# Optimization experiments

Measured on AMD Instinct MI355X. Metric: run time of the kernel, lower is better.

The kernel has to match this reference:

```python
import jax, jax.numpy as jnp
import numpy as np

HIDDEN = 2048
NUM_HEADS = 32
HEAD_DIM = 64
NUM_KV = 8
GROUP = NUM_HEADS // NUM_KV
SCALE = HEAD_DIM ** -0.5
ROPE_BASE = 10000.0


def apply_rope(t):
    # t: [B, H, S, D]; standard half-split rotary embedding
    S, D = t.shape[-2], t.shape[-1]
    inv_freq = 1.0 / (ROPE_BASE ** (jnp.arange(0, D, 2, dtype=jnp.float32) / D))  # [D/2]
    ang = jnp.arange(S, dtype=jnp.float32)[:, None] * inv_freq[None, :]           # [S, D/2]
    cos, sin = jnp.cos(ang), jnp.sin(ang)
    x1, x2 = t[..., : D // 2], t[..., D // 2 :]
    return jnp.concatenate([x1 * cos - x2 * sin, x2 * cos + x1 * sin], axis=-1)


def setup_inputs() -> dict:
    key = jax.random.key(0)
    ks = jax.random.split(key, 10)
    B, S = 2, 2048
    s_in = HIDDEN ** -0.5
    s_o = (NUM_HEADS * HEAD_DIM) ** -0.5
    return {
        "x": jax.random.normal(ks[0], (B, S, HIDDEN), jnp.float32),
        "Wq": jax.random.normal(ks[1], (NUM_HEADS * HEAD_DIM, HIDDEN), jnp.float32) * s_in,
        "bq": jnp.zeros((NUM_HEADS * HEAD_DIM,), jnp.float32),
        "Wk": jax.random.normal(ks[2], (NUM_KV * HEAD_DIM, HIDDEN), jnp.float32) * s_in,
        "bk": jnp.zeros((NUM_KV * HEAD_DIM,), jnp.float32),
        "Wv": jax.random.normal(ks[3], (NUM_KV * HEAD_DIM, HIDDEN), jnp.float32) * s_in,
        "bv": jnp.zeros((NUM_KV * HEAD_DIM,), jnp.float32),
        "Wo": jax.random.normal(ks[4], (HIDDEN, NUM_HEADS * HEAD_DIM), jnp.float32) * s_o,
        "bo": jnp.zeros((HIDDEN,), jnp.float32),
        "key_weights": jax.random.normal(ks[5], (NUM_HEADS,), jnp.float32),
    }


def reference(x, Wq, bq, Wk, bk, Wv, bv, Wo, bo, key_weights):
    B, S, _ = x.shape
    q = (x @ Wq.T + bq).reshape(B, S, NUM_HEADS, HEAD_DIM).transpose(0, 2, 1, 3)
    k = (x @ Wk.T + bk).reshape(B, S, NUM_KV, HEAD_DIM).transpose(0, 2, 1, 3)
    v = (x @ Wv.T + bv).reshape(B, S, NUM_KV, HEAD_DIM).transpose(0, 2, 1, 3)
    q = apply_rope(q)
    k = apply_rope(k)
    # group queries per KV head: [B, kv, g, S, D]
    qg = q.reshape(B, NUM_KV, GROUP, S, HEAD_DIM)
    scores = jnp.einsum("bkgsd,bktd->bkgst", qg, k) * SCALE
    scores = scores * key_weights.reshape(1, NUM_KV, GROUP, 1, 1)
    causal = jnp.tril(jnp.ones((S, S), bool))
    scores = jnp.where(causal, scores, -jnp.inf)
    a = jax.nn.softmax(scores, axis=-1)
    o = jnp.einsum("bkgst,bktd->bkgsd", a, v)  # [B, kv, g, S, D]
    o = o.reshape(B, NUM_HEADS, S, HEAD_DIM).transpose(0, 2, 1, 3).reshape(B, S, NUM_HEADS * HEAD_DIM)
    return o @ Wo.T + bo
```

## Files before the change

kernel.cpp:

```cpp
#include <hip/hip_runtime.h>
#include <stdint.h>

#define S_LEN 2048
#define HID   2048
#define NH    32
#define NKV   8
#define HD    64
#define BATCH 2
#define NROWS (BATCH * S_LEN)
#define QKVN  (NH*HD + 2*NKV*HD)

typedef unsigned short u16;
typedef __bf16 bf16_t;
typedef bf16_t bf16x8 __attribute__((ext_vector_type(8)));
typedef float  f32x4  __attribute__((ext_vector_type(4)));
typedef float  f32x16 __attribute__((ext_vector_type(16)));
typedef u16    u16x8  __attribute__((ext_vector_type(8)));

#define LOG2E 1.4426950408889634f

__device__ __forceinline__ u16 f2bf(float f) {
    union { float f; uint32_t u; } v; v.f = f;
    uint32_t u = v.u;
    return (u16)((u + 0x7fffu + ((u >> 16) & 1u)) >> 16);
}

__device__ __forceinline__ unsigned cvtpk(float a, float b) {
    unsigned r;
    asm("v_cvt_pk_bf16_f32 %0, %1, %2" : "=v"(r) : "v"(a), "v"(b));
    return r;
}

__device__ __forceinline__ void plswap(unsigned &a, unsigned &b) {
    asm volatile("v_permlane32_swap_b32 %0, %1" : "+v"(a), "+v"(b));
}

__device__ __forceinline__ void llds16(const void* g, void* l) {
    __builtin_amdgcn_global_load_lds(
        (const __attribute__((address_space(1))) void*)g,
        (__attribute__((address_space(3))) void*)l,
        16, 0, 0);
}

__device__ __forceinline__ unsigned swz(unsigned row) {
    return ((row ^ (row >> 2)) & 3u) << 4;
}

#define LGKM0() do { asm volatile("s_waitcnt lgkmcnt(0)" ::: "memory"); \
                     __builtin_amdgcn_sched_barrier(0); } while (0)
#define BAR()   __builtin_amdgcn_s_barrier()

#define CBAR(N) do { \
    asm volatile("s_waitcnt vmcnt(" #N ")" ::: "memory"); \
    __builtin_amdgcn_s_barrier(); \
    __builtin_amdgcn_sched_barrier(0); \
} while (0)

#define CVT_GROUPS 2359296
__global__ void prep_all(const float* __restrict__ x, const float* __restrict__ wq,
                         const float* __restrict__ wk, const float* __restrict__ wv,
                         const float* __restrict__ wo,
                         const float* __restrict__ bq, const float* __restrict__ bk,
                         const float* __restrict__ bv,
                         u16* __restrict__ xb, u16* __restrict__ wqkvb, u16* __restrict__ wob,
                         float* __restrict__ rtab, float* __restrict__ bqkv) {
    int e = blockIdx.x * 256 + threadIdx.x;
    if (e < CVT_GROUPS) {
        const float* s; u16* d; int o;
        if (e < 1048576)      { s = x;  d = xb;                 o = e; }
        else if (e < 1572864) { s = wq; d = wqkvb;              o = e - 1048576; }
        else if (e < 1703936) { s = wk; d = wqkvb + 2048*2048;  o = e - 1572864; }
        else if (e < 1835008) { s = wv; d = wqkvb + 2560*2048;  o = e - 1703936; }
        else                  { s = wo; d = wob;                o = e - 1835008; }
        const float4* sp = (const float4*)s;
        float4 a = sp[2*(size_t)o], b = sp[2*(size_t)o + 1];
        u16x8 r;
        r[0]=f2bf(a.x); r[1]=f2bf(a.y); r[2]=f2bf(a.z); r[3]=f2bf(a.w);
        r[4]=f2bf(b.x); r[5]=f2bf(b.y); r[6]=f2bf(b.z); r[7]=f2bf(b.w);
        *(u16x8*)(d + 8*(size_t)o) = r;
    } else if (e < CVT_GROUPS + 65536) {
        int idx = e - CVT_GROUPS;
        int i = idx & 31, s = idx >> 5;
        float invf = exp2f(-(float)i * (13.287712379549449f / 32.0f));
        float ang = (float)s * invf;
        float sn, cs;
        sincosf(ang, &sn, &cs);
        rtab[idx] = cs;
        rtab[S_LEN*32 + idx] = sn;
    } else if (e < CVT_GROUPS + 65536 + QKVN) {
        int i = e - CVT_GROUPS - 65536;
        bqkv[i] = (i < 2048) ? bq[i] : (i < 2560 ? bk[i - 2048] : bv[i - 2560]);
    }
}


__global__ __launch_bounds__(256, 2) void gemm_qkv(
    const u16* __restrict__ A, const u16* __restrict__ Bw,
    const float* __restrict__ bias, const float* __restrict__ rtab,
    const float* __restrict__ kw,
    u16* __restrict__ qpk, u16* __restrict__ kpk, u16* __restrict__ vlin)
{
    const int M = NROWS, N = QKVN, K = HID;
    const int nbn = N >> 8;
    const int nwg = (M >> 7) * nbn;
    int wg = blockIdx.x;
    wg = (wg & 7) * (nwg >> 3) + (wg >> 3);
    const int bm = wg / nbn, bn = wg % nbn;
    const int brow = bm << 7, bcol = bn << 8;

    __shared__ u16 sbuf[3][12288];

    const int t = threadIdx.x;
    const int lane = t & 63, wid = t >> 6;
    const int wr = wid >> 1, wn = wid & 1;
    const int lq = lane & 31, hi = lane >> 5;

    auto stageA = [&](int kt, int bi) {
        const int k0 = kt << 5;
        #pragma unroll
        for (int i = 0; i < 2; ++i) {
            const unsigned off = ((unsigned)t << 4) + ((unsigned)i << 12);
            const unsigned row = off >> 6;
            const unsigned scb = (off & 63) ^ swz(row);
            llds16(A + (size_t)(brow + row) * K + (k0 + (scb >> 1)), &sbuf[bi][0] + (off >> 1));
        }
        {
            const unsigned off = ((unsigned)t << 4);
            const unsigned row = off >> 6;
            const unsigned scb = (off & 63) ^ swz(row);
            llds16(Bw + (size_t)(bcol + row) * K + (k0 + (scb >> 1)), &sbuf[bi][4096] + (off >> 1));
        }
    };
    auto stageB = [&](int kt, int bi) {
        const int k0 = kt << 5;
        #pragma unroll
        for (int i = 1; i < 4; ++i) {
            const unsigned off = ((unsigned)t << 4) + ((unsigned)i << 12);
            const unsigned row = off >> 6;
            const unsigned scb = (off & 63) ^ swz(row);
            llds16(Bw + (size_t)(bcol + row) * K + (k0 + (scb >> 1)), &sbuf[bi][4096] + (off >> 1));
        }
    };

    f32x16 acc[2][4] = {};
    const int nk = K >> 5;

    stageA(0, 0); stageB(0, 0);
    stageA(1, 1); stageB(1, 1);
    asm volatile("s_waitcnt vmcnt(6)" ::: "memory");
    BAR();

    int cur = 0, st2 = 2;
    for (int kt = 0; kt < nk; ++kt) {
        const char* sA = (const char*)&sbuf[cur][0];
        const char* sB = (const char*)&sbuf[cur][4096];
        bf16x8 af[4], bfv[8];
        #pragma unroll
        for (int mt = 0; mt < 2; ++mt)
            #pragma unroll
            for (int s = 0; s < 2; ++s) {
                const unsigned row = wr*64 + mt*32 + lq;
                af[mt*2+s] = *(const bf16x8*)(sA + row*64 + ((unsigned)(32*s + 16*hi) ^ swz(row)));
            }
        #pragma unroll
        for (int nt = 0; nt < 2; ++nt)
            #pragma unroll
            for (int s = 0; s < 2; ++s) {
                const unsigned row = wn*128 + nt*32 + lq;
                bfv[nt*2+s] = *(const bf16x8*)(sB + row*64 + ((unsigned)(32*s + 16*hi) ^ swz(row)));
            }
        if (kt + 2 < nk) stageA(kt + 2, st2);
        BAR();
        LGKM0();
        __builtin_amdgcn_s_setprio(1);
        #pragma unroll
        for (int mt = 0; mt < 2; ++mt)
            #pragma unroll
            for (int nt = 0; nt < 2; ++nt)
                #pragma unroll
                for (int s = 0; s < 2; ++s)
                    acc[mt][nt] = __builtin_amdgcn_mfma_f32_32x32x16_bf16(af[mt*2+s], bfv[nt*2+s], acc[mt][nt], 0, 0, 0);
        __builtin_amdgcn_s_setprio(0);
        BAR();
        #pragma unroll
        for (int nt = 2; nt < 4; ++nt)
            #pragma unroll
            for (int s = 0; s < 2; ++s) {
                const unsigned row = wn*128 + nt*32 + lq;
                bfv[nt*2+s] = *(const bf16x8*)(sB + row*64 + ((unsigned)(32*s + 16*hi) ^ swz(row)));
            }
        if (kt + 2 < nk) stageB(kt + 2, st2);
        BAR();
        LGKM0();
        __builtin_amdgcn_s_setprio(1);
        #pragma unroll
        for (int mt = 0; mt < 2; ++mt)
            #pragma unroll
            for (int nt = 2; nt < 4; ++nt)
                #pragma unroll
                for (int s = 0; s < 2; ++s)
                    acc[mt][nt] = __builtin_amdgcn_mfma_f32_32x32x16_bf16(af[mt*2+s], bfv[nt*2+s], acc[mt][nt], 0, 0, 0);
        __builtin_amdgcn_s_setprio(0);
        if (kt + 2 < nk) {
            asm volatile("s_waitcnt vmcnt(6)" ::: "memory");
            BAR();
        } else if (kt + 1 < nk) {
            asm volatile("s_waitcnt vmcnt(0)" ::: "memory");
            BAR();
        }
        cur = (cur == 2) ? 0 : cur + 1;
        st2 = (st2 == 2) ? 0 : st2 + 1;
    }

    const int rowb = brow + wr*64;
    #pragma unroll
    for (int hg = 0; hg < 2; ++hg) {
        const int c64 = bcol + wn*128 + hg*64;
        const int hb  = c64 >> 6;
        if (hb < 40) {
            const bool isQ = hb < 32;
            const float sc = isQ ? (0.125f * LOG2E * kw[hb]) : 1.0f;
            u16* dst = isQ ? qpk : kpk;
            const int nheads = isQ ? 32 : 8;
            const int hloc = isQ ? hb : (hb - 32);
            const float b1 = bias[c64 + lq];
            const float b2 = bias[c64 + 32 + lq];
            #pragma unroll
            for (int mt = 0; mt < 2; ++mt) {
                #pragma unroll
                for (int r = 0; r < 16; ++r) {
                    const int row = rowb + mt*32 + (r & 3) + 8*(r >> 2) + 4*hi;
                    const int s = row & (S_LEN - 1);
                    const int bb = row >> 11;
                    const float x1 = acc[mt][2*hg][r] + b1;
                    const float x2 = acc[mt][2*hg + 1][r] + b2;
                    const float c = rtab[s*32 + lq];
                    const float sn = rtab[S_LEN*32 + s*32 + lq];
                    const size_t base = ((size_t)(bb*nheads + hloc)) * (S_LEN*64) + (size_t)s*64;
                    dst[base + lq]      = f2bf((x1*c - x2*sn) * sc);
                    dst[base + lq + 32] = f2bf((x2*c + x1*sn) * sc);
                }
            }
        } else {
            #pragma unroll
            for (int nn = 0; nn < 2; ++nn) {
                const int col = c64 + nn*32 + lq;
                const float bv = bias[col];
                #pragma unroll
                for (int mt = 0; mt < 2; ++mt)
                    #pragma unroll
                    for (int r = 0; r < 16; ++r) {
                        const int row = rowb + mt*32 + (r & 3) + 8*(r >> 2) + 4*hi;
                        vlin[(size_t)row * 512 + (col - 2560)] = f2bf(acc[mt][2*hg + nn][r] + bv);
                    }
            }
        }
    }
}

__global__ __launch_bounds__(256, 2) void gemm_bt(
    const u16* __restrict__ A, const u16* __restrict__ Bw,
    const float* __restrict__ bias, float* __restrict__ C,
    int M, int N, int K)
{
    const int nbn = N >> 8;
    const int nwg = (M >> 7) * nbn;
    int wg = blockIdx.x;
    wg = (wg & 7) * (nwg >> 3) + (wg >> 3);
    const int bm = wg / nbn, bn = wg % nbn;
    const int brow = bm << 7, bcol = bn << 8;

    __shared__ u16 sbuf[3][12288];

    const int t = threadIdx.x;
    const int lane = t & 63, wid = t >> 6;
    const int wr = wid >> 1, wn = wid & 1;
    const int lq = lane & 31, hi = lane >> 5;

    auto stageA = [&](int kt, int bi) {
        const int k0 = kt << 5;
        #pragma unroll
        for (int i = 0; i < 2; ++i) {
            const unsigned off = ((unsigned)t << 4) + ((unsigned)i << 12);
            const unsigned row = off >> 6;
            const unsigned scb = (off & 63) ^ swz(row);
            llds16(A + (size_t)(brow + row) * K + (k0 + (scb >> 1)), &sbuf[bi][0] + (off >> 1));
        }
        {
            const unsigned off = ((unsigned)t << 4);
            const unsigned row = off >> 6;
            const unsigned scb = (off & 63) ^ swz(row);
            llds16(Bw + (size_t)(bcol + row) * K + (k0 + (scb >> 1)), &sbuf[bi][4096] + (off >> 1));
        }
    };
    auto stageB = [&](int kt, int bi) {
        const int k0 = kt << 5;
        #pragma unroll
        for (int i = 1; i < 4; ++i) {
            const unsigned off = ((unsigned)t << 4) + ((unsigned)i << 12);
            const unsigned row = off >> 6;
            const unsigned scb = (off & 63) ^ swz(row);
            llds16(Bw + (size_t)(bcol + row) * K + (k0 + (scb >> 1)), &sbuf[bi][4096] + (off >> 1));
        }
    };

    f32x16 acc[2][4] = {};
    const int nk = K >> 5;

    stageA(0, 0); stageB(0, 0);
    stageA(1, 1); stageB(1, 1);
    asm volatile("s_waitcnt vmcnt(6)" ::: "memory");
    BAR();

    int cur = 0, st2 = 2;
    for (int kt = 0; kt < nk; ++kt) {
        const char* sA = (const char*)&sbuf[cur][0];
        const char* sB = (const char*)&sbuf[cur][4096];
        bf16x8 af[4], bfv[8];
        #pragma unroll
        for (int mt = 0; mt < 2; ++mt)
            #pragma unroll
            for (int s = 0; s < 2; ++s) {
                const unsigned row = wr*64 + mt*32 + lq;
                af[mt*2+s] = *(const bf16x8*)(sA + row*64 + ((unsigned)(32*s + 16*hi) ^ swz(row)));
            }
        #pragma unroll
        for (int nt = 0; nt < 2; ++nt)
            #pragma unroll
            for (int s = 0; s < 2; ++s) {
                const unsigned row = wn*128 + nt*32 + lq;
                bfv[nt*2+s] = *(const bf16x8*)(sB + row*64 + ((unsigned)(32*s + 16*hi) ^ swz(row)));
            }
        if (kt + 2 < nk) stageA(kt + 2, st2);
        BAR();
        LGKM0();
        __builtin_amdgcn_s_setprio(1);
        #pragma unroll
        for (int mt = 0; mt < 2; ++mt)
            #pragma unroll
            for (int nt = 0; nt < 2; ++nt)
                #pragma unroll
                for (int s = 0; s < 2; ++s)
                    acc[mt][nt] = __builtin_amdgcn_mfma_f32_32x32x16_bf16(af[mt*2+s], bfv[nt*2+s], acc[mt][nt], 0, 0, 0);
        __builtin_amdgcn_s_setprio(0);
        BAR();
        #pragma unroll
        for (int nt = 2; nt < 4; ++nt)
            #pragma unroll
            for (int s = 0; s < 2; ++s) {
                const unsigned row = wn*128 + nt*32 + lq;
                bfv[nt*2+s] = *(const bf16x8*)(sB + row*64 + ((unsigned)(32*s + 16*hi) ^ swz(row)));
            }
        if (kt + 2 < nk) stageB(kt + 2, st2);
        BAR();
        LGKM0();
        __builtin_amdgcn_s_setprio(1);
        #pragma unroll
        for (int mt = 0; mt < 2; ++mt)
            #pragma unroll
            for (int nt = 2; nt < 4; ++nt)
                #pragma unroll
                for (int s = 0; s < 2; ++s)
                    acc[mt][nt] = __builtin_amdgcn_mfma_f32_32x32x16_bf16(af[mt*2+s], bfv[nt*2+s], acc[mt][nt], 0, 0, 0);
        __builtin_amdgcn_s_setprio(0);
        if (kt + 2 < nk) {
            asm volatile("s_waitcnt vmcnt(6)" ::: "memory");
            BAR();
        } else if (kt + 1 < nk) {
            asm volatile("s_waitcnt vmcnt(0)" ::: "memory");
            BAR();
        }
        cur = (cur == 2) ? 0 : cur + 1;
        st2 = (st2 == 2) ? 0 : st2 + 1;
    }

    #pragma unroll
    for (int mt = 0; mt < 2; ++mt)
        #pragma unroll
        for (int nt = 0; nt < 4; ++nt) {
            const int col = bcol + wn*128 + nt*32 + lq;
            const float bv = bias[col];
            #pragma unroll
            for (int r = 0; r < 16; ++r) {
                const int row = brow + wr*64 + mt*32 + (r & 3) + 8*(r >> 2) + 4*hi;
                C[(size_t)row * N + col] = acc[mt][nt][r] + bv;
            }
        }
}

__global__ void pack_vt(const u16* __restrict__ vlin, u16* __restrict__ vtb) {
    __shared__ u16 tile[64][67];
    const int st = blockIdx.x;
    const int bk = blockIdx.y;
    const int t = threadIdx.x;
    const int b = bk >> 3, kvh = bk & 7;
    const int r = t >> 2, cg = (t & 3) << 4;
    const u16* src = vlin + ((size_t)(b*S_LEN + st*64 + r)) * 512 + kvh*64 + cg;
    #pragma unroll
    for (int j = 0; j < 16; ++j) tile[r][cg + j] = src[j];
    __syncthreads();
    const int d = t >> 2, sg = (t & 3) << 4;
    u16* dst = vtb + ((size_t)(bk*64 + d)) * S_LEN + st*64 + sg;
    #pragma unroll
    for (int j = 0; j < 16; ++j) dst[j] = tile[sg + j][d];
}

__global__ __launch_bounds__(512, 4) void attn_fwd(
    const u16* __restrict__ Q,
    const u16* __restrict__ Kk,
    const u16* __restrict__ Vt,
    u16* __restrict__ O)
{
    __shared__ u16 sK[3][64 * 64];
    __shared__ u16 sV[3][64 * 64];

    const int t = threadIdx.x;
    const int lane = t & 63, wid = t >> 6;
    const int hi = lane >> 5, lq = lane & 31;
    const int bid = blockIdx.x;
    const int qb = (bid < 256) ? (7 - (bid >> 6)) : ((bid >> 6) - 4);
    const int bh = bid & 63;
    const int b = bh >> 5, h = bh & 31;
    const int kvh = h >> 2;

    const u16* Kp = Kk + ((size_t)(b*NKV + kvh)) * (S_LEN * 64);
    const u16* Vp = Vt + ((size_t)(b*NKV + kvh)) * (64 * S_LEN);

    const int q0w = qb*256 + wid*32;
    const int qg  = q0w + lq;

    const u16* Qrow = Q + (((size_t)bh) * S_LEN + qg) * 64 + 8*hi;
    bf16x8 qf[4];
    #pragma unroll
    for (int kd = 0; kd < 4; ++kd)
        qf[kd] = *(const bf16x8*)(Qrow + 16*kd);

    f32x16 accO0 = {}, accO1 = {};
    float m_run = 0.f, l_run = 0.f;

    const int ntB = 4*qb + 4;
    const int tmax_w = (q0w + 31) >> 6;

    auto stageKV = [&](int kt, int bi) {
        const int kv = kt << 6;
        const unsigned row = t >> 3, cb = (t & 7) << 4;
        const unsigned scb = cb ^ ((row & 7) << 4);
        llds16(Kp + (size_t)(kv + row) * 64 + (scb >> 1), &sK[bi][0] + t*8);
        llds16(Vp + (size_t)row * S_LEN + kv + (scb >> 1), &sV[bi][0] + t*8);
    };

    stageKV(0, 0);
    stageKV(1, 1);
    int cur = 0, st2 = 2;

    for (int tt = 0; tt < ntB; ++tt) {
        if (tt < ntB - 1) CBAR(2); else CBAR(0);
        if (tt + 2 < ntB) stageKV(tt + 2, st2);
        if (tt <= tmax_w) {
            const int kv0 = tt * 64;
            const float nm = -m_run;
            f32x16 s0, s1;
            #pragma unroll
            for (int r = 0; r < 16; ++r) { s0[r] = nm; s1[r] = nm; }
            __builtin_amdgcn_s_setprio(1);
            #pragma unroll
            for (int kd = 0; kd < 4; ++kd) {
                const unsigned bc = ((unsigned)(32*kd + 16*hi)) ^ ((lq & 7) << 4);
                bf16x8 k0 = *(const bf16x8*)((const char*)&sK[cur][0] + lq*128 + bc);
                bf16x8 k1 = *(const bf16x8*)((const char*)&sK[cur][0] + (32 + lq)*128 + bc);
                s0 = __builtin_amdgcn_mfma_f32_32x32x16_bf16(k0, qf[kd], s0, 0, 0, 0);
                s1 = __builtin_amdgcn_mfma_f32_32x32x16_bf16(k1, qf[kd], s1, 0, 0, 0);
            }
            __builtin_amdgcn_s_setprio(0);
            if (kv0 + 63 > q0w) {
                #pragma unroll
                for (int r = 0; r < 16; ++r) {
                    const int kvg = kv0 + (r & 3) + 8*(r >> 2) + 4*hi;
                    if (kvg > qg)      s0[r] = -INFINITY;
                    if (kvg + 32 > qg) s1[r] = -INFINITY;
                }
            }
            float mx[8];
            #pragma unroll
            for (int r = 0; r < 8; ++r)
                mx[r] = fmaxf(fmaxf(s0[r], s0[r+8]), fmaxf(s1[r], s1[r+8]));
            float tm = fmaxf(fmaxf(fmaxf(mx[0], mx[1]), fmaxf(mx[2], mx[3])),
                             fmaxf(fmaxf(mx[4], mx[5]), fmaxf(mx[6], mx[7])));
            tm = fmaxf(tm, __shfl_xor(tm, 32));
            if (!__all(tm <= 8.0f)) {
                const float dd = fmaxf(tm, 0.f);
                const float al = __builtin_amdgcn_exp2f(-dd);
                m_run += dd;
                l_run *= al;
                #pragma unroll
                for (int r = 0; r < 16; ++r) { accO0[r] *= al; accO1[r] *= al; }
                #pragma unroll
                for (int r = 0; r < 16; ++r) { s0[r] -= dd; s1[r] -= dd; }
            }
            #pragma unroll
            for (int r = 0; r < 16; ++r) {
                s0[r] = __builtin_amdgcn_exp2f(s0[r]);
                s1[r] = __builtin_amdgcn_exp2f(s1[r]);
            }
            float sm[8];
            #pragma unroll
            for (int r = 0; r < 8; ++r)
                sm[r] = (s0[r] + s0[r+8]) + (s1[r] + s1[r+8]);
            float rs = ((sm[0]+sm[1]) + (sm[2]+sm[3])) + ((sm[4]+sm[5]) + (sm[6]+sm[7]));
            rs += __shfl_xor(rs, 32);
            l_run += rs;

            #pragma unroll
            for (int ks = 0; ks < 4; ++ks) {
                const f32x16& e = (ks & 2) ? s1 : s0;
                const int rb = (ks & 1) * 8;
                unsigned x0 = cvtpk(e[rb + 0], e[rb + 1]);
                unsigned x1 = cvtpk(e[rb + 2], e[rb + 3]);
                unsigned y0 = cvtpk(e[rb + 4], e[rb + 5]);
                unsigned y1 = cvtpk(e[rb + 6], e[rb + 7]);
                plswap(x0, y0);
                plswap(x1, y1);
                union { unsigned u[4]; bf16x8 v; } pb;
                pb.u[0] = x0; pb.u[1] = x1; pb.u[2] = y0; pb.u[3] = y1;
                const unsigned bc = ((unsigned)(32*ks + 16*hi)) ^ ((lq & 7) << 4);
                bf16x8 v0 = *(const bf16x8*)((const char*)&sV[cur][0] + lq*128 + bc);
                bf16x8 v1 = *(const bf16x8*)((const char*)&sV[cur][0] + (32 + lq)*128 + bc);
                __builtin_amdgcn_s_setprio(1);
                accO0 = __builtin_amdgcn_mfma_f32_32x32x16_bf16(v0, pb.v, accO0, 0, 0, 0);
                accO1 = __builtin_amdgcn_mfma_f32_32x32x16_bf16(v1, pb.v, accO1, 0, 0, 0);
                __builtin_amdgcn_s_setprio(0);
            }
        }
        cur = (cur == 2) ? 0 : cur + 1;
        st2 = (st2 == 2) ? 0 : st2 + 1;
    }

    const float inv = 1.0f / l_run;
    u16* orow = O + (((size_t)(b * S_LEN) + q0w + lq)) * (NH*HD) + h*64;
    #pragma unroll
    for (int g = 0; g < 4; ++g) {
        uint2 w0, w1;
        w0.x = cvtpk(accO0[4*g + 0] * inv, accO0[4*g + 1] * inv);
        w0.y = cvtpk(accO0[4*g + 2] * inv, accO0[4*g + 3] * inv);
        *(uint2*)(orow + 8*g + 4*hi) = w0;
        w1.x = cvtpk(accO1[4*g + 0] * inv, accO1[4*g + 1] * inv);
        w1.y = cvtpk(accO1[4*g + 2] * inv, accO1[4*g + 3] * inv);
        *(uint2*)(orow + 32 + 8*g + 4*hi) = w1;
    }
}

extern "C" void kernel_launch(void* const* d_in, const int* in_sizes, int n_in,
                              void* d_out, int out_size, void* d_ws, size_t ws_size,
                              hipStream_t stream) {
    const float* x  = (const float*)d_in[0];
    const float* Wq = (const float*)d_in[1];
    const float* bq = (const float*)d_in[2];
    const float* Wk = (const float*)d_in[3];
    const float* bk = (const float*)d_in[4];
    const float* Wv = (const float*)d_in[5];
    const float* bv = (const float*)d_in[6];
    const float* Wo = (const float*)d_in[7];
    const float* bo = (const float*)d_in[8];
    const float* kw = (const float*)d_in[9];

    uint8_t* ws = (uint8_t*)d_ws;
    u16*   xb    = (u16*)(ws);
    u16*   wqkvb = (u16*)(ws + 16777216);
    u16*   wob   = (u16*)(ws + 29360128);
    u16*   qpk   = (u16*)(ws + 37748736);
    u16*   kpk   = (u16*)(ws + 54525952);
    u16*   vlin  = (u16*)(ws + 58720256);
    u16*   vtb   = (u16*)(ws + 62914560);
    u16*   ob    = (u16*)(ws + 67108864);
    float* bqkv  = (float*)(ws + 83886080);
    float* rtab  = (float*)(ws + 83898368);

    prep_all<<<9484, 256, 0, stream>>>(x, Wq, Wk, Wv, Wo, bq, bk, bv,
                                       xb, wqkvb, wob, rtab, bqkv);

    gemm_qkv<<<384, 256, 0, stream>>>(xb, wqkvb, bqkv, rtab, kw, qpk, kpk, vlin);

    pack_vt<<<dim3(32, 16), 256, 0, stream>>>(vlin, vtb);

    attn_fwd<<<dim3(512), dim3(512), 0, stream>>>(qpk, kpk, vtb, ob);

    gemm_bt<<<256, 256, 0, stream>>>(ob, wob, bo, (float*)d_out, NROWS, HID, HID);

    (void)in_sizes; (void)n_in; (void)out_size; (void)ws_size;
}
```

Before: 187.3 us.

## Restructure GEMM main loop to one barrier per k-step with partial lgkm waits

Both GEMM kernels (QKV projection and output projection) now issue all LDS fragment reads for a k-tile up front, then the whole prefetch for tile k+2, and wait with lgkmcnt(4) so the first half of the MFMAs can start while the second half of the B fragments is still in flight. The three-buffer ring now uses a single vmcnt wait plus barrier at the top of each iteration, replacing the three or four barriers per iteration. This is meant to cut barrier stalls and overlap LDS reads with MFMA. It raises register pressure because all B fragments are live at once, and it relies on the three-stage buffer to keep the prefetch for k+2 from overwriting data other waves are still reading.

```diff
diff --git a/kernel.cpp b/kernel.cpp
--- a/kernel.cpp
+++ b/kernel.cpp
@@ -46,8 +46,7 @@
     return ((row ^ (row >> 2)) & 3u) << 4;
 }
 
-#define LGKM0() do { asm volatile("s_waitcnt lgkmcnt(0)" ::: "memory"); \
-                     __builtin_amdgcn_sched_barrier(0); } while (0)
+#define SB()    __builtin_amdgcn_sched_barrier(0)
 #define BAR()   __builtin_amdgcn_s_barrier()
 
 #define CBAR(N) do { \
@@ -115,7 +114,7 @@
     const int wr = wid >> 1, wn = wid & 1;
     const int lq = lane & 31, hi = lane >> 5;
 
-    auto stageA = [&](int kt, int bi) {
+    auto stageAll = [&](int kt, int bi) {
         const int k0 = kt << 5;
         #pragma unroll
         for (int i = 0; i < 2; ++i) {
@@ -124,17 +123,8 @@
             const unsigned scb = (off & 63) ^ swz(row);
             llds16(A + (size_t)(brow + row) * K + (k0 + (scb >> 1)), &sbuf[bi][0] + (off >> 1));
         }
-        {
-            const unsigned off = ((unsigned)t << 4);
-            const unsigned row = off >> 6;
-            const unsigned scb = (off & 63) ^ swz(row);
-            llds16(Bw + (size_t)(bcol + row) * K + (k0 + (scb >> 1)), &sbuf[bi][4096] + (off >> 1));
-        }
-    };
-    auto stageB = [&](int kt, int bi) {
-        const int k0 = kt << 5;
-        #pragma unroll
-        for (int i = 1; i < 4; ++i) {
+        #pragma unroll
+        for (int i = 0; i < 4; ++i) {
             const unsigned off = ((unsigned)t << 4) + ((unsigned)i << 12);
             const unsigned row = off >> 6;
             const unsigned scb = (off & 63) ^ swz(row);
@@ -145,13 +135,14 @@
     f32x16 acc[2][4] = {};
     const int nk = K >> 5;
 
-    stageA(0, 0); stageB(0, 0);
-    stageA(1, 1); stageB(1, 1);
-    asm volatile("s_waitcnt vmcnt(6)" ::: "memory");
-    BAR();
-
+    stageAll(0, 0);
+    stageAll(1, 1);
     int cur = 0, st2 = 2;
     for (int kt = 0; kt < nk; ++kt) {
+        if (kt + 1 < nk) asm volatile("s_waitcnt vmcnt(6)" ::: "memory");
+        else             asm volatile("s_waitcnt vmcnt(0)" ::: "memory");
+        BAR();
+        SB();
         const char* sA = (const char*)&sbuf[cur][0];
         const char* sB = (const char*)&sbuf[cur][4096];
         bf16x8 af[4], bfv[8];
@@ -169,9 +160,18 @@
                 const unsigned row = wn*128 + nt*32 + lq;
                 bfv[nt*2+s] = *(const bf16x8*)(sB + row*64 + ((unsigned)(32*s + 16*hi) ^ swz(row)));
             }
-        if (kt + 2 < nk) stageA(kt + 2, st2);
-        BAR();
-        LGKM0();
+        SB();
+        #pragma unroll
+        for (int nt = 2; nt < 4; ++nt)
+            #pragma unroll
+            for (int s = 0; s < 2; ++s) {
+                const unsigned row = wn*128 + nt*32 + lq;
+                bfv[nt*2+s] = *(const bf16x8*)(sB + row*64 + ((unsigned)(32*s + 16*hi) ^ swz(row)));
+            }
+        SB();
+        if (kt + 2 < nk) stageAll(kt + 2, st2);
+        asm volatile("s_waitcnt lgkmcnt(4)" ::: "memory");
+        SB();
         __builtin_amdgcn_s_setprio(1);
         #pragma unroll
         for (int mt = 0; mt < 2; ++mt)
@@ -181,17 +181,8 @@
                 for (int s = 0; s < 2; ++s)
                     acc[mt][nt] = __builtin_amdgcn_mfma_f32_32x32x16_bf16(af[mt*2+s], bfv[nt*2+s], acc[mt][nt], 0, 0, 0);
         __builtin_amdgcn_s_setprio(0);
-        BAR();
-        #pragma unroll
-        for (int nt = 2; nt < 4; ++nt)
-            #pragma unroll
-            for (int s = 0; s < 2; ++s) {
-                const unsigned row = wn*128 + nt*32 + lq;
-                bfv[nt*2+s] = *(const bf16x8*)(sB + row*64 + ((unsigned)(32*s + 16*hi) ^ swz(row)));
-            }
-        if (kt + 2 < nk) stageB(kt + 2, st2);
-        BAR();
-        LGKM0();
+        asm volatile("s_waitcnt lgkmcnt(0)" ::: "memory");
+        SB();
         __builtin_amdgcn_s_setprio(1);
         #pragma unroll
         for (int mt = 0; mt < 2; ++mt)
@@ -201,13 +192,6 @@
                 for (int s = 0; s < 2; ++s)
                     acc[mt][nt] = __builtin_amdgcn_mfma_f32_32x32x16_bf16(af[mt*2+s], bfv[nt*2+s], acc[mt][nt], 0, 0, 0);
         __builtin_amdgcn_s_setprio(0);
-        if (kt + 2 < nk) {
-            asm volatile("s_waitcnt vmcnt(6)" ::: "memory");
-            BAR();
-        } else if (kt + 1 < nk) {
-            asm volatile("s_waitcnt vmcnt(0)" ::: "memory");
-            BAR();
-        }
         cur = (cur == 2) ? 0 : cur + 1;
         st2 = (st2 == 2) ? 0 : st2 + 1;
     }
@@ -277,7 +261,7 @@
     const int wr = wid >> 1, wn = wid & 1;
     const int lq = lane & 31, hi = lane >> 5;
 
-    auto stageA = [&](int kt, int bi) {
+    auto stageAll = [&](int kt, int bi) {
         const int k0 = kt << 5;
         #pragma unroll
         for (int i = 0; i < 2; ++i) {
@@ -286,17 +270,8 @@
             const unsigned scb = (off & 63) ^ swz(row);
             llds16(A + (size_t)(brow + row) * K + (k0 + (scb >> 1)), &sbuf[bi][0] + (off >> 1));
         }
-        {
-            const unsigned off = ((unsigned)t << 4);
-            const unsigned row = off >> 6;
-            const unsigned scb = (off & 63) ^ swz(row);
-            llds16(Bw + (size_t)(bcol + row) * K + (k0 + (scb >> 1)), &sbuf[bi][4096] + (off >> 1));
-        }
-    };
-    auto stageB = [&](int kt, int bi) {
-        const int k0 = kt << 5;
-        #pragma unroll
-        for (int i = 1; i < 4; ++i) {
+        #pragma unroll
+        for (int i = 0; i < 4; ++i) {
             const unsigned off = ((unsigned)t << 4) + ((unsigned)i << 12);
             const unsigned row = off >> 6;
             const unsigned scb = (off & 63) ^ swz(row);
@@ -307,13 +282,14 @@
     f32x16 acc[2][4] = {};
     const int nk = K >> 5;
 
-    stageA(0, 0); stageB(0, 0);
-    stageA(1, 1); stageB(1, 1);
-    asm volatile("s_waitcnt vmcnt(6)" ::: "memory");
-    BAR();
-
+    stageAll(0, 0);
+    stageAll(1, 1);
     int cur = 0, st2 = 2;
     for (int kt = 0; kt < nk; ++kt) {
+        if (kt + 1 < nk) asm volatile("s_waitcnt vmcnt(6)" ::: "memory");
+        else             asm volatile("s_waitcnt vmcnt(0)" ::: "memory");
+        BAR();
+        SB();
         const char* sA = (const char*)&sbuf[cur][0];
         const char* sB = (const char*)&sbuf[cur][4096];
         bf16x8 af[4], bfv[8];
@@ -331,9 +307,18 @@
                 const unsigned row = wn*128 + nt*32 + lq;
                 bfv[nt*2+s] = *(const bf16x8*)(sB + row*64 + ((unsigned)(32*s + 16*hi) ^ swz(row)));
             }
-        if (kt + 2 < nk) stageA(kt + 2, st2);
-        BAR();
-        LGKM0();
+        SB();
+        #pragma unroll
+        for (int nt = 2; nt < 4; ++nt)
+            #pragma unroll
+            for (int s = 0; s < 2; ++s) {
+                const unsigned row = wn*128 + nt*32 + lq;
+                bfv[nt*2+s] = *(const bf16x8*)(sB + row*64 + ((unsigned)(32*s + 16*hi) ^ swz(row)));
+            }
+        SB();
+        if (kt + 2 < nk) stageAll(kt + 2, st2);
+        asm volatile("s_waitcnt lgkmcnt(4)" ::: "memory");
+        SB();
         __builtin_amdgcn_s_setprio(1);
         #pragma unroll
         for (int mt = 0; mt < 2; ++mt)
@@ -343,17 +328,8 @@
                 for (int s = 0; s < 2; ++s)
                     acc[mt][nt] = __builtin_amdgcn_mfma_f32_32x32x16_bf16(af[mt*2+s], bfv[nt*2+s], acc[mt][nt], 0, 0, 0);
         __builtin_amdgcn_s_setprio(0);
-        BAR();
-        #pragma unroll
-        for (int nt = 2; nt < 4; ++nt)
-            #pragma unroll
-            for (int s = 0; s < 2; ++s) {
-                const unsigned row = wn*128 + nt*32 + lq;
-                bfv[nt*2+s] = *(const bf16x8*)(sB + row*64 + ((unsigned)(32*s + 16*hi) ^ swz(row)));
-            }
-        if (kt + 2 < nk) stageB(kt + 2, st2);
-        BAR();
-        LGKM0();
+        asm volatile("s_waitcnt lgkmcnt(0)" ::: "memory");
+        SB();
         __builtin_amdgcn_s_setprio(1);
         #pragma unroll
         for (int mt = 0; mt < 2; ++mt)
@@ -363,13 +339,6 @@
                 for (int s = 0; s < 2; ++s)
                     acc[mt][nt] = __builtin_amdgcn_mfma_f32_32x32x16_bf16(af[mt*2+s], bfv[nt*2+s], acc[mt][nt], 0, 0, 0);
         __builtin_amdgcn_s_setprio(0);
-        if (kt + 2 < nk) {
-            asm volatile("s_waitcnt vmcnt(6)" ::: "memory");
-            BAR();
-        } else if (kt + 1 < nk) {
-            asm volatile("s_waitcnt vmcnt(0)" ::: "memory");
-            BAR();
-        }
         cur = (cur == 2) ? 0 : cur + 1;
         st2 = (st2 == 2) ? 0 : st2 + 1;
     }
```

Measured after the change: 188.7 us. About the same (+0.8%).
